# Kernel optimization log

Measured on AMD Instinct MI355X. Metric: run time of the kernel, lower is better.

## Reference

```python
import jax, jax.numpy as jnp
import numpy as np

N_NODES = 10000
N_EDGES = 160000
IN_C, HID_C, OUT_C = 256, 512, 256
DROP_P = 0.5


def setup_inputs() -> dict:
    key = jax.random.key(0)
    ks = jax.random.split(key, 6)
    tensor = jax.random.normal(ks[0], (N_NODES, IN_C), dtype=jnp.float32)
    edge_index = jax.random.randint(ks[1], (2, N_EDGES), 0, N_NODES, dtype=jnp.int64)
    # Glorot-ish init for GCNConv linear weights, zero bias (PyG default bias init is zeros)
    W1 = jax.random.normal(ks[2], (IN_C, HID_C), dtype=jnp.float32) * (1.0 / np.sqrt(IN_C))
    b1 = jnp.zeros((HID_C,), dtype=jnp.float32)
    W2 = jax.random.normal(ks[3], (HID_C, OUT_C), dtype=jnp.float32) * (1.0 / np.sqrt(HID_C))
    b2 = jnp.zeros((OUT_C,), dtype=jnp.float32)
    return {"tensor": tensor, "edge_index": edge_index, "W1": W1, "b1": b1, "W2": W2, "b2": b2}


def _gcn_layer(x, W, b, src, dst, n_nodes):
    # x' = D^{-1/2} (A + I) D^{-1/2} X W + b  (PyG GCNConv, add_self_loops=True)
    xw = x @ W                                             # [N, C_out]
    deg = jax.ops.segment_sum(jnp.ones(src.shape[0], xw.dtype), dst,
                              num_segments=n_nodes)        # includes self-loops -> deg >= 1
    dinv = jax.lax.rsqrt(deg)
    norm = dinv[src] * dinv[dst]                           # [E+N]
    msg = xw[src] * norm[:, None]                          # gather + normalize
    out = jax.ops.segment_sum(msg, dst, num_segments=n_nodes)  # scatter-add
    return out + b


def _dropout(x, key, p):
    keep = jax.random.bernoulli(key, 1.0 - p, x.shape)
    return jnp.where(keep, x / (1.0 - p), jnp.zeros((), x.dtype))


def reference(tensor, edge_index, W1, b1, W2, b2):
    n = tensor.shape[0]
    src, dst = edge_index[0], edge_index[1]
    loops = jnp.arange(n, dtype=src.dtype)
    src_f = jnp.concatenate([src, loops])
    dst_f = jnp.concatenate([dst, loops])

    dk1, dk2 = jax.random.split(jax.random.key(42))
    h = _gcn_layer(tensor, W1, b1, src_f, dst_f, n)
    h = jax.nn.relu(h)
    h = _dropout(h, dk1, DROP_P)
    h = _gcn_layer(h, W2, b2, src_f, dst_f, n)
    h = jax.nn.relu(h)
    h = _dropout(h, dk2, DROP_P)
    return h
```

## Files before the change

### kernel.cpp

```cpp
#include <hip/hip_runtime.h>
#include <stdint.h>


#define C_IN 256
#define C_HID 512
#define C_OUT 256

typedef unsigned short ushort_t;
typedef __bf16 bf16x8 __attribute__((ext_vector_type(8)));
typedef float floatx4 __attribute__((ext_vector_type(4)));

typedef __attribute__((address_space(1))) const void g1_void;
typedef __attribute__((address_space(3))) void l3_void;

__device__ __forceinline__ void gll16(const ushort_t* g, ushort_t* l) {
  __builtin_amdgcn_global_load_lds((g1_void*)g, (l3_void*)l, 16, 0, 0);
}

__host__ __device__ __forceinline__ void tf_rounds(unsigned& x0, unsigned& x1,
                                                   unsigned k0, unsigned k1) {
  unsigned k2 = k0 ^ k1 ^ 0x1BD11BDAu;
#define ROT(r) { x0 += x1; x1 = (x1 << r) | (x1 >> (32 - r)); x1 ^= x0; }
  x0 += k0; x1 += k1;
  ROT(13) ROT(15) ROT(26) ROT(6)
  x0 += k1; x1 += k2 + 1u;
  ROT(17) ROT(29) ROT(16) ROT(24)
  x0 += k2; x1 += k0 + 2u;
  ROT(13) ROT(15) ROT(26) ROT(6)
  x0 += k0; x1 += k1 + 3u;
  ROT(17) ROT(29) ROT(16) ROT(24)
  x0 += k1; x1 += k2 + 4u;
  ROT(13) ROT(15) ROT(26) ROT(6)
  x0 += k2; x1 += k0 + 5u;
#undef ROT
}

__device__ __forceinline__ float drop_scale(unsigned j, unsigned k0, unsigned k1) {
  unsigned x0 = 0u, x1 = j;
  tf_rounds(x0, x1, k0, k1);
  unsigned bits = x0 ^ x1;
  float u = __uint_as_float((bits >> 9) | 0x3f800000u) - 1.0f;
  return (u < 0.5f) ? 2.0f : 0.0f;
}

__device__ __forceinline__ ushort_t f2bf(float f) {
  unsigned u = __float_as_uint(f);
  unsigned r = (u + 0x7fffu + ((u >> 16) & 1u)) >> 16;
  return (ushort_t)r;
}
__device__ __forceinline__ float bf2f(ushort_t h) {
  return __uint_as_float(((unsigned)h) << 16);
}

__global__ __launch_bounds__(256) void k_setup(const unsigned* __restrict__ raw,
                                               unsigned* __restrict__ flag,
                                               int* __restrict__ cnt, int N, int NB,
                                               const float* __restrict__ W1,
                                               const float* __restrict__ W2,
                                               ushort_t* __restrict__ h1,
                                               ushort_t* __restrict__ l1,
                                               ushort_t* __restrict__ h2,
                                               ushort_t* __restrict__ l2) {
  int b = blockIdx.x, t = threadIdx.x;
  if (b < NB) {
    int i = b * 256 + t;
    if (i < N) cnt[i] = 0;
    return;
  }
  if (b == NB) {
    __shared__ unsigned sh[256];
    unsigned acc = 0;
    for (int i = 1 + 2 * t; i < 8192; i += 512) acc |= raw[i];
    sh[t] = acc;
    __syncthreads();
    for (int s = 128; s > 0; s >>= 1) {
      if (t < s) sh[t] |= sh[t + s];
      __syncthreads();
    }
    if (t == 0) *flag = (sh[0] == 0u) ? 1u : 0u;
    return;
  }
  int idx = (b - NB - 1) * 256 + t;
  const int S1 = C_IN * C_HID;
  if (idx >= S1 + C_HID * C_OUT) return;
  const float* W; ushort_t *hi, *lo; int K, Nn, li;
  if (idx < S1) { W = W1; hi = h1; lo = l1; K = C_IN; Nn = C_HID; li = idx; }
  else { W = W2; hi = h2; lo = l2; K = C_HID; Nn = C_OUT; li = idx - S1; }
  int k = li / Nn, n = li - k * Nn;
  float v = W[li];
  ushort_t h = f2bf(v);
  hi[(size_t)n * K + k] = h;
  lo[(size_t)n * K + k] = f2bf(v - bf2f(h));
}

__global__ __launch_bounds__(256) void k_hist(const void* __restrict__ raw,
                                              const unsigned* __restrict__ flag,
                                              int* __restrict__ cnt, int E) {
  int e = blockIdx.x * 256 + threadIdx.x;
  if (e >= E) return;
  int d;
  if (*flag) d = (int)((const long long*)raw)[E + e];
  else       d = ((const int*)raw)[E + e];
  atomicAdd(&cnt[d], 1);
}

__global__ __launch_bounds__(1024) void k_scan(const int* __restrict__ cnt,
                                               int* __restrict__ roff,
                                               int* __restrict__ cursor,
                                               float* __restrict__ dinv,
                                               int n, int E) {
  __shared__ int wsum[16];
  __shared__ int sbase;
  int t = threadIdx.x;
  int lane = t & 63, w = t >> 6;
  if (t == 0) sbase = 0;
  __syncthreads();
  for (int c0 = 0; c0 < n; c0 += 1024) {
    int i = c0 + t;
    int v = (i < n) ? cnt[i] : 0;
    int sc = v;
#pragma unroll
    for (int d = 1; d < 64; d <<= 1) {
      int u = __shfl_up(sc, d);
      if (lane >= d) sc += u;
    }
    if (lane == 63) wsum[w] = sc;
    __syncthreads();
    int wpre = 0;
#pragma unroll
    for (int k = 0; k < 16; ++k) wpre += (k < w) ? wsum[k] : 0;
    int base = sbase;
    if (i < n) {
      int excl = base + wpre + sc - v;
      roff[i] = excl;
      cursor[i] = excl;
      dinv[i] = rsqrtf((float)(v + 1));
    }
    __syncthreads();
    if (t == 1023) sbase = base + wpre + sc;
    __syncthreads();
  }
  if (t == 0) roff[n] = E;
}

__global__ __launch_bounds__(256) void k_scatter(const void* __restrict__ raw,
                                                 const unsigned* __restrict__ flag,
                                                 int* __restrict__ cursor,
                                                 int* __restrict__ csr, int E) {
  int e = blockIdx.x * 256 + threadIdx.x;
  if (e >= E) return;
  int s, d;
  if (*flag) {
    s = (int)((const long long*)raw)[e];
    d = (int)((const long long*)raw)[E + e];
  } else {
    s = ((const int*)raw)[e];
    d = ((const int*)raw)[E + e];
  }
  int slot = atomicAdd(&cursor[d], 1);
  csr[slot] = s;
}

template <int EPI, int PRE>
__global__ __launch_bounds__(256) void k_gather4(const int* __restrict__ roff,
                                                 const int* __restrict__ csr,
                                                 const float* __restrict__ dinv,
                                                 const float* __restrict__ x,
                                                 const float* __restrict__ bias,
                                                 void* __restrict__ o1,
                                                 void* __restrict__ o2,
                                                 unsigned dk0, unsigned dk1) {
  int g = threadIdx.x >> 6;
  int tg = threadIdx.x & 63;
  int node = blockIdx.x * 4 + g;
  float dd = dinv[node];
  const float4* xr = (const float4*)x;
  float4 v = xr[(size_t)node * 64 + tg];
  float4 acc;
  if (PRE) acc = v;
  else acc = make_float4(dd * v.x, dd * v.y, dd * v.z, dd * v.w);
  int p = roff[node], end = roff[node + 1];
  int s[8];
  bool have = (p + 8 <= end);
  if (have) {
#pragma unroll
    for (int q = 0; q < 8; ++q) s[q] = csr[p + q];
  }
  while (have) {
    int sn[8];
    bool haven = (p + 16 <= end);
    if (haven) {
#pragma unroll
      for (int q = 0; q < 8; ++q) sn[q] = csr[p + 8 + q];
    }
    float4 r[8];
#pragma unroll
    for (int q = 0; q < 8; ++q) r[q] = xr[(size_t)s[q] * 64 + tg];
    if (PRE) {
#pragma unroll
      for (int q = 0; q < 8; ++q) {
        acc.x += r[q].x; acc.y += r[q].y; acc.z += r[q].z; acc.w += r[q].w;
      }
    } else {
      float w[8];
#pragma unroll
      for (int q = 0; q < 8; ++q) w[q] = dinv[s[q]];
#pragma unroll
      for (int q = 0; q < 8; ++q) {
        acc.x += w[q] * r[q].x; acc.y += w[q] * r[q].y;
        acc.z += w[q] * r[q].z; acc.w += w[q] * r[q].w;
      }
    }
    p += 8;
#pragma unroll
    for (int q = 0; q < 8; ++q) s[q] = sn[q];
    have = haven;
  }
  for (; p + 4 <= end; p += 4) {
    int s0 = csr[p], s1 = csr[p + 1], s2 = csr[p + 2], s3 = csr[p + 3];
    float4 a = xr[(size_t)s0 * 64 + tg];
    float4 b = xr[(size_t)s1 * 64 + tg];
    float4 c = xr[(size_t)s2 * 64 + tg];
    float4 d = xr[(size_t)s3 * 64 + tg];
    if (PRE) {
      acc.x += a.x + b.x + c.x + d.x;
      acc.y += a.y + b.y + c.y + d.y;
      acc.z += a.z + b.z + c.z + d.z;
      acc.w += a.w + b.w + c.w + d.w;
    } else {
      float w0 = dinv[s0], w1 = dinv[s1], w2 = dinv[s2], w3 = dinv[s3];
      acc.x += w0 * a.x + w1 * b.x + w2 * c.x + w3 * d.x;
      acc.y += w0 * a.y + w1 * b.y + w2 * c.y + w3 * d.y;
      acc.z += w0 * a.z + w1 * b.z + w2 * c.z + w3 * d.z;
      acc.w += w0 * a.w + w1 * b.w + w2 * c.w + w3 * d.w;
    }
  }
  for (; p < end; ++p) {
    int s0 = csr[p];
    float4 a = xr[(size_t)s0 * 64 + tg];
    if (PRE) {
      acc.x += a.x; acc.y += a.y; acc.z += a.z; acc.w += a.w;
    } else {
      float w0 = dinv[s0];
      acc.x += w0 * a.x; acc.y += w0 * a.y; acc.z += w0 * a.z; acc.w += w0 * a.w;
    }
  }
  acc.x *= dd; acc.y *= dd; acc.z *= dd; acc.w *= dd;
  if (EPI) {
    float4 bb = ((const float4*)bias)[tg];
    acc.x = fmaxf(acc.x + bb.x, 0.0f);
    acc.y = fmaxf(acc.y + bb.y, 0.0f);
    acc.z = fmaxf(acc.z + bb.z, 0.0f);
    acc.w = fmaxf(acc.w + bb.w, 0.0f);
    unsigned jb = (unsigned)node * 256u + (unsigned)tg * 4u;
    acc.x *= drop_scale(jb + 0u, dk0, dk1);
    acc.y *= drop_scale(jb + 1u, dk0, dk1);
    acc.z *= drop_scale(jb + 2u, dk0, dk1);
    acc.w *= drop_scale(jb + 3u, dk0, dk1);
    ((float4*)o1)[(size_t)node * 64 + tg] = acc;
  } else {
    ushort_t h0 = f2bf(acc.x), h1 = f2bf(acc.y), h2 = f2bf(acc.z), h3 = f2bf(acc.w);
    ushort4 hv = make_ushort4(h0, h1, h2, h3);
    ushort4 lv = make_ushort4(f2bf(acc.x - bf2f(h0)), f2bf(acc.y - bf2f(h1)),
                              f2bf(acc.z - bf2f(h2)), f2bf(acc.w - bf2f(h3)));
    ((ushort4*)o1)[(size_t)node * 64 + tg] = hv;
    ((ushort4*)o2)[(size_t)node * 64 + tg] = lv;
  }
}

__global__ __launch_bounds__(256, 2) void k_gemm12(
    const ushort_t* __restrict__ Ahi, const ushort_t* __restrict__ Alo,
    const ushort_t* __restrict__ B1h, const ushort_t* __restrict__ B1l,
    const ushort_t* __restrict__ B2h, const ushort_t* __restrict__ B2l,
    const float* __restrict__ b1, const float* __restrict__ dinv,
    float* __restrict__ hw2, int M, unsigned dk0, unsigned dk1) {
  __shared__ __attribute__((aligned(16))) ushort_t sBh[2][8192], sBl[2][8192];
  __shared__ __attribute__((aligned(16))) ushort_t sHh[4096], sHl[4096];
  const int t = threadIdx.x;
  const int lane = t & 63, wave = t >> 6;
  const int wm = wave & 1, wn = wave >> 1;
  const int quad = lane >> 4, l16 = lane & 15;
  const int row0 = blockIdx.x * 32;
  const int rA = wm * 16 + l16;

  bf16x8 Ah[8], Al[8];
  {
    const int ga = min(row0 + rA, M - 1);
    const ushort_t* pa = Ahi + (size_t)ga * 256 + quad * 8;
    const ushort_t* pl = Alo + (size_t)ga * 256 + quad * 8;
#pragma unroll
    for (int k8 = 0; k8 < 8; ++k8) {
      Ah[k8] = *(const bf16x8*)(pa + k8 * 32);
      Al[k8] = *(const bf16x8*)(pl + k8 * 32);
    }
  }
  float bpre[4][4];
#pragma unroll
  for (int cb = 0; cb < 4; ++cb)
#pragma unroll
    for (int j = 0; j < 4; ++j)
      bpre[cb][j] = b1[cb * 128 + wn * 64 + j * 16 + l16];
#pragma unroll
  for (int k8 = 0; k8 < 8; ++k8)
    asm volatile("" :: "v"(Ah[k8]), "v"(Al[k8]));
#pragma unroll
  for (int cb = 0; cb < 4; ++cb)
    asm volatile("" :: "v"(bpre[cb][0]), "v"(bpre[cb][1]),
                       "v"(bpre[cb][2]), "v"(bpre[cb][3]));

#define STG(bh_, bl_, Kd_, colb_, kb_, c_) {                                   \
    _Pragma("unroll")                                                          \
    for (int i_ = 0; i_ < 4; ++i_) {                                           \
      int slab_ = wave * 4 + i_;                                               \
      int row_ = slab_ * 8 + (lane >> 3);                                      \
      int kch_ = (((lane & 7) ^ (row_ & 7)) * 8);                              \
      gll16(bh_ + (size_t)(colb_ + row_) * Kd_ + (kb_) + kch_,                 \
            &sBh[c_][slab_ * 512]);                                            \
      gll16(bl_ + (size_t)(colb_ + row_) * Kd_ + (kb_) + kch_,                 \
            &sBl[c_][slab_ * 512]);                                            \
    } }

  STG(B1h, B1l, 256, 0, 0, 0)
  asm volatile("s_waitcnt vmcnt(0)\n\ts_barrier" ::: "memory");

  floatx4 acc2[2][4] = {};
  int c = 0;
  for (int cb = 0; cb < 4; ++cb) {
    floatx4 acc1[4] = {};
#pragma unroll
    for (int k2 = 0; k2 < 4; ++k2) {
      if (k2 < 3) { STG(B1h, B1l, 256, cb * 128, (k2 + 1) * 64, c ^ 1) }
      else        { STG(B2h, B2l, 512, 0, cb * 128, c ^ 1) }
      asm volatile("s_waitcnt vmcnt(8)\n\ts_barrier" ::: "memory");
#pragma unroll
      for (int kk = 0; kk < 2; ++kk) {
        bf16x8 ah = Ah[k2 * 2 + kk], al = Al[k2 * 2 + kk];
#pragma unroll
        for (int j = 0; j < 4; ++j) {
          int rb = wn * 64 + j * 16 + l16;
          int ob = rb * 64 + (((kk * 4 + quad) ^ (rb & 7)) * 8);
          bf16x8 bh = *(const bf16x8*)&sBh[c][ob];
          bf16x8 bl = *(const bf16x8*)&sBl[c][ob];
          acc1[j] = __builtin_amdgcn_mfma_f32_16x16x32_bf16(ah, bh, acc1[j], 0, 0, 0);
          acc1[j] = __builtin_amdgcn_mfma_f32_16x16x32_bf16(ah, bl, acc1[j], 0, 0, 0);
          acc1[j] = __builtin_amdgcn_mfma_f32_16x16x32_bf16(al, bh, acc1[j], 0, 0, 0);
        }
      }
      asm volatile("s_barrier" ::: "memory");
      c ^= 1;
    }
#pragma unroll
    for (int j = 0; j < 4; ++j) {
      int kc = wn * 64 + j * 16 + l16;
      int gc = cb * 128 + kc;
      float bb = bpre[cb][j];
#pragma unroll
      for (int reg = 0; reg < 4; ++reg) {
        int row = wm * 16 + quad * 4 + reg;
        float v = fmaxf(acc1[j][reg] + bb, 0.0f);
        v *= drop_scale((unsigned)(row0 + row) * 512u + (unsigned)gc, dk0, dk1);
        ushort_t h = f2bf(v);
        int idx = row * 128 + (((kc >> 3) ^ (row & 7)) * 8) + (kc & 7);
        sHh[idx] = h;
        sHl[idx] = f2bf(v - bf2f(h));
      }
    }
    asm volatile("s_waitcnt lgkmcnt(0)\n\ts_barrier" ::: "memory");
    bf16x8 hh[4], hl[4];
#pragma unroll
    for (int kc2 = 0; kc2 < 4; ++kc2) {
      int oh = rA * 128 + (((kc2 * 4 + quad) ^ (rA & 7)) * 8);
      hh[kc2] = *(const bf16x8*)&sHh[oh];
      hl[kc2] = *(const bf16x8*)&sHl[oh];
    }
#pragma unroll
    for (int s2 = 0; s2 < 4; ++s2) {
      const int ph = s2 >> 1, kk2 = s2 & 1;
      bool staged = true;
      if (s2 < 3) {
        const int sn = s2 + 1;
        STG(B2h, B2l, 512, (sn >> 1) * 128, cb * 128 + (sn & 1) * 64, c ^ 1)
      } else if (cb < 3) {
        STG(B1h, B1l, 256, (cb + 1) * 128, 0, c ^ 1)
      } else {
        staged = false;
      }
      if (staged) asm volatile("s_waitcnt vmcnt(8)\n\ts_barrier" ::: "memory");
      else        asm volatile("s_waitcnt vmcnt(0)\n\ts_barrier" ::: "memory");
#pragma unroll
      for (int kk = 0; kk < 2; ++kk) {
        bf16x8 ah = hh[kk2 * 2 + kk], al = hl[kk2 * 2 + kk];
#pragma unroll
        for (int j = 0; j < 4; ++j) {
          int rb = wn * 64 + j * 16 + l16;
          int ob = rb * 64 + (((kk * 4 + quad) ^ (rb & 7)) * 8);
          bf16x8 bh = *(const bf16x8*)&sBh[c][ob];
          bf16x8 bl = *(const bf16x8*)&sBl[c][ob];
          acc2[ph][j] = __builtin_amdgcn_mfma_f32_16x16x32_bf16(ah, bh, acc2[ph][j], 0, 0, 0);
          acc2[ph][j] = __builtin_amdgcn_mfma_f32_16x16x32_bf16(ah, bl, acc2[ph][j], 0, 0, 0);
          acc2[ph][j] = __builtin_amdgcn_mfma_f32_16x16x32_bf16(al, bh, acc2[ph][j], 0, 0, 0);
        }
      }
      asm volatile("s_barrier" ::: "memory");
      c ^= 1;
    }
  }
#undef STG
#pragma unroll
  for (int ph = 0; ph < 2; ++ph) {
#pragma unroll
    for (int j = 0; j < 4; ++j) {
      int gc = ph * 128 + wn * 64 + j * 16 + l16;
#pragma unroll
      for (int reg = 0; reg < 4; ++reg) {
        int gr = row0 + wm * 16 + quad * 4 + reg;
        if (gr < M) hw2[(size_t)gr * 256 + gc] = acc2[ph][j][reg] * dinv[gr];
      }
    }
  }
}

extern "C" void kernel_launch(void* const* d_in, const int* in_sizes, int n_in,
                              void* d_out, int out_size, void* d_ws, size_t ws_size,
                              hipStream_t stream) {
  const float* x  = (const float*)d_in[0];
  const void*  ei = d_in[1];
  const float* W1 = (const float*)d_in[2];
  const float* b1 = (const float*)d_in[3];
  const float* W2 = (const float*)d_in[4];
  const float* b2 = (const float*)d_in[5];
  float* out = (float*)d_out;

  const int N = in_sizes[0] / C_IN;
  const int E = in_sizes[1] / 2;
  const int NB = (N + 255) / 256;

  unsigned a0 = 0u, a1 = 0u, b0 = 0u, b1k = 1u;
  tf_rounds(a0, a1, 0u, 42u);
  tf_rounds(b0, b1k, 0u, 42u);

  uintptr_t base = (uintptr_t)d_ws;
  unsigned*  flag   = (unsigned*)base;
  int*       cnt    = (int*)(base + 16 * 1024);
  int*       roff   = (int*)(base + 64 * 1024);
  int*       cursor = (int*)(base + 128 * 1024);
  float*     dinv   = (float*)(base + 192 * 1024);
  int*       csr    = (int*)(base + 2u * 1024 * 1024);
  ushort_t*  Ahi    = (ushort_t*)(base + 4u  * 1024 * 1024);
  ushort_t*  Alo    = (ushort_t*)(base + 10u * 1024 * 1024);
  float*     hw2    = (float*)(base + 38u * 1024 * 1024);
  ushort_t*  W1thi  = (ushort_t*)(base + 49u * 1024 * 1024);
  ushort_t*  W1tlo  = (ushort_t*)(base + 49u * 1024 * 1024 + 512 * 1024);
  ushort_t*  W2thi  = (ushort_t*)(base + 50u * 1024 * 1024);
  ushort_t*  W2tlo  = (ushort_t*)(base + 50u * 1024 * 1024 + 512 * 1024);

  dim3 b256(256);
  const int WCB = (C_IN * C_HID + C_HID * C_OUT + 255) / 256;

  k_setup<<<dim3(NB + 1 + WCB), b256, 0, stream>>>((const unsigned*)ei, flag, cnt,
                                                   N, NB, W1, W2,
                                                   W1thi, W1tlo, W2thi, W2tlo);
  k_hist<<<dim3((E + 255) / 256), b256, 0, stream>>>(ei, flag, cnt, E);
  k_scan<<<dim3(1), dim3(1024), 0, stream>>>(cnt, roff, cursor, dinv, N, E);
  k_scatter<<<dim3((E + 255) / 256), b256, 0, stream>>>(ei, flag, cursor, csr, E);
  k_gather4<0, 0><<<dim3(N / 4), b256, 0, stream>>>(roff, csr, dinv, x, nullptr,
                                                    Ahi, Alo, 0u, 0u);
  k_gemm12<<<dim3((N + 31) / 32), b256, 0, stream>>>(
      Ahi, Alo, W1thi, W1tlo, W2thi, W2tlo, b1, dinv, hw2, N, a0, a1);
  k_gather4<1, 1><<<dim3(N / 4), b256, 0, stream>>>(roff, csr, dinv, hw2, b2,
                                                    out, nullptr, b0, b1k);
}
```

Baseline: 205.7 us.

## Split fused GEMM block across eight waves with single-buffered LDS staging

The fused two-layer GEMM kernel now runs with 512 threads per block instead of 256. Each wave computes half as many output columns, so accumulator and bias register counts shrink. The double-buffered weight tiles in LDS with asynchronous prefetch of the next tile are replaced by one buffer, loaded between two __syncthreads barriers before each compute step. This halves LDS use and spreads the MFMA work across more waves, but global-to-LDS loads no longer overlap with compute.

```diff
diff --git a/kernel.cpp b/kernel.cpp
--- a/kernel.cpp
+++ b/kernel.cpp
@@ -268,13 +268,13 @@
   }
 }
 
-__global__ __launch_bounds__(256, 2) void k_gemm12(
+__global__ __launch_bounds__(512) void k_gemm12(
     const ushort_t* __restrict__ Ahi, const ushort_t* __restrict__ Alo,
     const ushort_t* __restrict__ B1h, const ushort_t* __restrict__ B1l,
     const ushort_t* __restrict__ B2h, const ushort_t* __restrict__ B2l,
     const float* __restrict__ b1, const float* __restrict__ dinv,
     float* __restrict__ hw2, int M, unsigned dk0, unsigned dk1) {
-  __shared__ __attribute__((aligned(16))) ushort_t sBh[2][8192], sBl[2][8192];
+  __shared__ __attribute__((aligned(16))) ushort_t sBh[8192], sBl[8192];
   __shared__ __attribute__((aligned(16))) ushort_t sHh[4096], sHl[4096];
   const int t = threadIdx.x;
   const int lane = t & 63, wave = t >> 6;
@@ -294,64 +294,57 @@
       Al[k8] = *(const bf16x8*)(pl + k8 * 32);
     }
   }
-  float bpre[4][4];
+  float bpre[4][2];
 #pragma unroll
   for (int cb = 0; cb < 4; ++cb)
 #pragma unroll
-    for (int j = 0; j < 4; ++j)
-      bpre[cb][j] = b1[cb * 128 + wn * 64 + j * 16 + l16];
+    for (int j = 0; j < 2; ++j)
+      bpre[cb][j] = b1[cb * 128 + wn * 32 + j * 16 + l16];
 #pragma unroll
   for (int k8 = 0; k8 < 8; ++k8)
     asm volatile("" :: "v"(Ah[k8]), "v"(Al[k8]));
 #pragma unroll
   for (int cb = 0; cb < 4; ++cb)
-    asm volatile("" :: "v"(bpre[cb][0]), "v"(bpre[cb][1]),
-                       "v"(bpre[cb][2]), "v"(bpre[cb][3]));
-
-#define STG(bh_, bl_, Kd_, colb_, kb_, c_) {                                   \
+    asm volatile("" :: "v"(bpre[cb][0]), "v"(bpre[cb][1]));
+
+#define STG(bh_, bl_, Kd_, colb_, kb_) {                                       \
     _Pragma("unroll")                                                          \
-    for (int i_ = 0; i_ < 4; ++i_) {                                           \
-      int slab_ = wave * 4 + i_;                                               \
+    for (int i_ = 0; i_ < 2; ++i_) {                                           \
+      int slab_ = wave * 2 + i_;                                               \
       int row_ = slab_ * 8 + (lane >> 3);                                      \
       int kch_ = (((lane & 7) ^ (row_ & 7)) * 8);                              \
       gll16(bh_ + (size_t)(colb_ + row_) * Kd_ + (kb_) + kch_,                 \
-            &sBh[c_][slab_ * 512]);                                            \
+            &sBh[slab_ * 512]);                                                \
       gll16(bl_ + (size_t)(colb_ + row_) * Kd_ + (kb_) + kch_,                 \
-            &sBl[c_][slab_ * 512]);                                            \
+            &sBl[slab_ * 512]);                                                \
     } }
 
-  STG(B1h, B1l, 256, 0, 0, 0)
-  asm volatile("s_waitcnt vmcnt(0)\n\ts_barrier" ::: "memory");
-
-  floatx4 acc2[2][4] = {};
-  int c = 0;
+  floatx4 acc2[2][2] = {};
   for (int cb = 0; cb < 4; ++cb) {
-    floatx4 acc1[4] = {};
+    floatx4 acc1[2] = {};
 #pragma unroll
     for (int k2 = 0; k2 < 4; ++k2) {
-      if (k2 < 3) { STG(B1h, B1l, 256, cb * 128, (k2 + 1) * 64, c ^ 1) }
-      else        { STG(B2h, B2l, 512, 0, cb * 128, c ^ 1) }
-      asm volatile("s_waitcnt vmcnt(8)\n\ts_barrier" ::: "memory");
+      __syncthreads();
+      STG(B1h, B1l, 256, cb * 128, k2 * 64)
+      __syncthreads();
 #pragma unroll
       for (int kk = 0; kk < 2; ++kk) {
         bf16x8 ah = Ah[k2 * 2 + kk], al = Al[k2 * 2 + kk];
 #pragma unroll
-        for (int j = 0; j < 4; ++j) {
-          int rb = wn * 64 + j * 16 + l16;
+        for (int j = 0; j < 2; ++j) {
+          int rb = wn * 32 + j * 16 + l16;
           int ob = rb * 64 + (((kk * 4 + quad) ^ (rb & 7)) * 8);
-          bf16x8 bh = *(const bf16x8*)&sBh[c][ob];
-          bf16x8 bl = *(const bf16x8*)&sBl[c][ob];
+          bf16x8 bh = *(const bf16x8*)&sBh[ob];
+          bf16x8 bl = *(const bf16x8*)&sBl[ob];
           acc1[j] = __builtin_amdgcn_mfma_f32_16x16x32_bf16(ah, bh, acc1[j], 0, 0, 0);
           acc1[j] = __builtin_amdgcn_mfma_f32_16x16x32_bf16(ah, bl, acc1[j], 0, 0, 0);
           acc1[j] = __builtin_amdgcn_mfma_f32_16x16x32_bf16(al, bh, acc1[j], 0, 0, 0);
         }
       }
-      asm volatile("s_barrier" ::: "memory");
-      c ^= 1;
-    }
-#pragma unroll
-    for (int j = 0; j < 4; ++j) {
-      int kc = wn * 64 + j * 16 + l16;
+    }
+#pragma unroll
+    for (int j = 0; j < 2; ++j) {
+      int kc = wn * 32 + j * 16 + l16;
       int gc = cb * 128 + kc;
       float bb = bpre[cb][j];
 #pragma unroll
@@ -365,7 +358,7 @@
         sHl[idx] = f2bf(v - bf2f(h));
       }
     }
-    asm volatile("s_waitcnt lgkmcnt(0)\n\ts_barrier" ::: "memory");
+    __syncthreads();
     bf16x8 hh[4], hl[4];
 #pragma unroll
     for (int kc2 = 0; kc2 < 4; ++kc2) {
@@ -376,41 +369,31 @@
 #pragma unroll
     for (int s2 = 0; s2 < 4; ++s2) {
       const int ph = s2 >> 1, kk2 = s2 & 1;
-      bool staged = true;
-      if (s2 < 3) {
-        const int sn = s2 + 1;
-        STG(B2h, B2l, 512, (sn >> 1) * 128, cb * 128 + (sn & 1) * 64, c ^ 1)
-      } else if (cb < 3) {
-        STG(B1h, B1l, 256, (cb + 1) * 128, 0, c ^ 1)
-      } else {
-        staged = false;
-      }
-      if (staged) asm volatile("s_waitcnt vmcnt(8)\n\ts_barrier" ::: "memory");
-      else        asm volatile("s_waitcnt vmcnt(0)\n\ts_barrier" ::: "memory");
+      __syncthreads();
+      STG(B2h, B2l, 512, ph * 128, cb * 128 + kk2 * 64)
+      __syncthreads();
 #pragma unroll
       for (int kk = 0; kk < 2; ++kk) {
         bf16x8 ah = hh[kk2 * 2 + kk], al = hl[kk2 * 2 + kk];
 #pragma unroll
-        for (int j = 0; j < 4; ++j) {
-          int rb = wn * 64 + j * 16 + l16;
+        for (int j = 0; j < 2; ++j) {
+          int rb = wn * 32 + j * 16 + l16;
           int ob = rb * 64 + (((kk * 4 + quad) ^ (rb & 7)) * 8);
-          bf16x8 bh = *(const bf16x8*)&sBh[c][ob];
-          bf16x8 bl = *(const bf16x8*)&sBl[c][ob];
+          bf16x8 bh = *(const bf16x8*)&sBh[ob];
+          bf16x8 bl = *(const bf16x8*)&sBl[ob];
           acc2[ph][j] = __builtin_amdgcn_mfma_f32_16x16x32_bf16(ah, bh, acc2[ph][j], 0, 0, 0);
           acc2[ph][j] = __builtin_amdgcn_mfma_f32_16x16x32_bf16(ah, bl, acc2[ph][j], 0, 0, 0);
           acc2[ph][j] = __builtin_amdgcn_mfma_f32_16x16x32_bf16(al, bh, acc2[ph][j], 0, 0, 0);
         }
       }
-      asm volatile("s_barrier" ::: "memory");
-      c ^= 1;
     }
   }
 #undef STG
 #pragma unroll
   for (int ph = 0; ph < 2; ++ph) {
 #pragma unroll
-    for (int j = 0; j < 4; ++j) {
-      int gc = ph * 128 + wn * 64 + j * 16 + l16;
+    for (int j = 0; j < 2; ++j) {
+      int gc = ph * 128 + wn * 32 + j * 16 + l16;
 #pragma unroll
       for (int reg = 0; reg < 4; ++reg) {
         int gr = row0 + wm * 16 + quad * 4 + reg;
@@ -465,7 +448,7 @@
   k_scatter<<<dim3((E + 255) / 256), b256, 0, stream>>>(ei, flag, cursor, csr, E);
   k_gather4<0, 0><<<dim3(N / 4), b256, 0, stream>>>(roff, csr, dinv, x, nullptr,
                                                     Ahi, Alo, 0u, 0u);
-  k_gemm12<<<dim3((N + 31) / 32), b256, 0, stream>>>(
+  k_gemm12<<<dim3((N + 31) / 32), dim3(512), 0, stream>>>(
       Ahi, Alo, W1thi, W1tlo, W2thi, W2tlo, b1, dinv, hw2, N, a0, a1);
   k_gather4<1, 1><<<dim3(N / 4), b256, 0, stream>>>(roff, csr, dinv, hw2, b2,
                                                     out, nullptr, b0, b1k);
```

Measured after the change: 227.4 us. 1.11x slower.
